# Kernel tuning notes

Hardware: AMD Instinct MI355X
Metric: run time of the kernel (lower is better)

Reference implementation:

```python
import jax, jax.numpy as jnp
import numpy as np

N_NODES = 40000
N_EDGES = 640000
D_IN = 512
D_OUT = 128


def setup_inputs() -> dict:
    key = jax.random.key(0)
    k_x, k_w, k_a, k_v, k_r, k_c = jax.random.split(key, 6)
    # Xavier-uniform bound for Linear(in=512, out=128)
    bound = float(np.sqrt(6.0 / (D_IN + D_OUT)))
    x = jax.random.normal(k_x, (N_NODES, D_IN), dtype=jnp.float32)
    weight = jax.random.uniform(k_w, (D_OUT, D_IN), dtype=jnp.float32,
                                minval=-bound, maxval=bound)
    bias = jnp.zeros((D_OUT,), dtype=jnp.float32)
    # PReLU default init is 0.25 (single shared slope)
    alpha = jnp.full((1,), 0.25, dtype=jnp.float32)
    edge_val = jax.random.uniform(k_v, (N_EDGES,), dtype=jnp.float32)
    edge_row = jax.random.randint(k_r, (N_EDGES,), 0, N_NODES, dtype=jnp.int32)
    edge_col = jax.random.randint(k_c, (N_EDGES,), 0, N_NODES, dtype=jnp.int32)
    return {"x": x, "weight": weight, "bias": bias, "alpha": alpha,
            "edge_val": edge_val, "edge_row": edge_row, "edge_col": edge_col}


def reference(x, weight, bias, alpha, edge_val, edge_row, edge_col):
    # seq = fc_1(input): [N, D_out]
    seq = jnp.einsum('ni,oi->no', x, weight)
    # torch.spmm(adj, seq) with adj in COO form:
    # out[r] = sum over edges (r, c, v) of v * seq[c]
    msgs = edge_val[:, None] * seq[edge_col]          # [E, D_out]
    agg = jax.ops.segment_sum(msgs, edge_row, num_segments=x.shape[0])
    agg = agg + bias
    # PReLU with a single shared slope alpha
    return jnp.where(agg > 0, agg, alpha[0] * agg)
```

## Files before the change

kernel.cpp:

```cpp
#include <hip/hip_runtime.h>
#include <hip/hip_bf16.h>

#define N_NODES 40000
#define N_EDGES 640000
#define D_IN 512
#define D_OUT 128
#define BM 128
#define BK 64
#define CAP 128
#define NB_GE 313
#define EPT 4
#define NB_SC 625

typedef __attribute__((ext_vector_type(4))) float f32x4;
typedef __attribute__((ext_vector_type(8))) short bf16x8;
typedef __attribute__((ext_vector_type(4))) unsigned short us4;

static __device__ __forceinline__ unsigned short f2bf(float f) {
    unsigned int u = __float_as_uint(f);
    unsigned int r = u + 0x7fffu + ((u >> 16) & 1u);
    return (unsigned short)(r >> 16);
}

__global__ void zero_kernel(int* __restrict__ p, int n) {
    int i = blockIdx.x * blockDim.x + threadIdx.x;
    if (i < n) p[i] = 0;
}

__global__ __launch_bounds__(256) void fused_kernel(
    const float* __restrict__ x, const float* __restrict__ w,
    unsigned short* __restrict__ seq,
    const int* __restrict__ erow, const int* __restrict__ ecol,
    const float* __restrict__ eval, int* __restrict__ cursor,
    float2* __restrict__ bucket)
{
    if (blockIdx.x >= NB_GE) {
        const int base = (blockIdx.x - NB_GE) * (256 * EPT) + threadIdx.x;
        int r[EPT], c[EPT];
        float v[EPT];
        #pragma unroll
        for (int k = 0; k < EPT; k++) {
            int e = base + k * 256;
            r[k] = erow[e]; c[k] = ecol[e]; v[k] = eval[e];
        }
        int slot[EPT];
        #pragma unroll
        for (int k = 0; k < EPT; k++) slot[k] = atomicAdd(&cursor[r[k]], 1);
        #pragma unroll
        for (int k = 0; k < EPT; k++)
            bucket[(size_t)r[k] * CAP + slot[k]] = make_float2(v[k], __int_as_float(c[k]));
        return;
    }

    __shared__ unsigned short As[BM * BK];
    __shared__ unsigned short Bs[D_OUT * BK];

    const int tid = threadIdx.x;
    const int lane = tid & 63;
    const int wv = tid >> 6;
    const int block_row = blockIdx.x * BM;
    const int srow = tid >> 3;
    const int scol = (tid & 7) * 8;

    f32x4 ra[4][2], rb[4][2];

    auto issue_loads = [&](int k0) {
        #pragma unroll
        for (int p = 0; p < 4; ++p) {
            int gr = block_row + srow + p * 32; if (gr >= N_NODES) gr = N_NODES - 1;
            const float* sa = x + (size_t)gr * D_IN + k0 + scol;
            ra[p][0] = *(const f32x4*)sa;
            ra[p][1] = *(const f32x4*)(sa + 4);
            const float* sb = w + (size_t)(srow + p * 32) * D_IN + k0 + scol;
            rb[p][0] = *(const f32x4*)sb;
            rb[p][1] = *(const f32x4*)(sb + 4);
        }
    };

    f32x4 acc[2][8];
    #pragma unroll
    for (int i = 0; i < 2; i++)
        #pragma unroll
        for (int j = 0; j < 8; j++)
            acc[i][j] = f32x4{0.f, 0.f, 0.f, 0.f};

    issue_loads(0);

    for (int kt = 0; kt < D_IN / BK; ++kt) {
        __syncthreads();
        #pragma unroll
        for (int p = 0; p < 4; ++p) {
            int r = srow + p * 32;
            us4 h0, h1, g0, g1;
            #pragma unroll
            for (int q = 0; q < 4; q++) {
                h0[q] = f2bf(ra[p][0][q]); h1[q] = f2bf(ra[p][1][q]);
                g0[q] = f2bf(rb[p][0][q]); g1[q] = f2bf(rb[p][1][q]);
            }
            int off = (r * (BK * 2) + scol * 2) ^ ((r & 7) << 4);
            *(us4*)((char*)As + off)     = h0;
            *(us4*)((char*)As + off + 8) = h1;
            *(us4*)((char*)Bs + off)     = g0;
            *(us4*)((char*)Bs + off + 8) = g1;
        }
        if (kt < D_IN / BK - 1) issue_loads((kt + 1) * BK);
        __syncthreads();

        #pragma unroll
        for (int ks = 0; ks < 2; ++ks) {
            const int kb = ks * 32 + (lane >> 4) * 8;
            bf16x8 a[2], b[8];
            #pragma unroll
            for (int m = 0; m < 2; m++) {
                int r = wv * 32 + m * 16 + (lane & 15);
                int off = (r * (BK * 2) + kb * 2) ^ ((r & 7) << 4);
                a[m] = *(const bf16x8*)((const char*)As + off);
            }
            #pragma unroll
            for (int n = 0; n < 8; n++) {
                int r = n * 16 + (lane & 15);
                int off = (r * (BK * 2) + kb * 2) ^ ((r & 7) << 4);
                b[n] = *(const bf16x8*)((const char*)Bs + off);
            }
            #pragma unroll
            for (int m = 0; m < 2; m++)
                #pragma unroll
                for (int n = 0; n < 8; n++)
                    acc[m][n] = __builtin_amdgcn_mfma_f32_16x16x32_bf16(a[m], b[n], acc[m][n], 0, 0, 0);
        }
    }

    #pragma unroll
    for (int m = 0; m < 2; m++) {
        #pragma unroll
        for (int r = 0; r < 4; r++) {
            int grow = block_row + wv * 32 + m * 16 + (lane >> 4) * 4 + r;
            if (grow < N_NODES) {
                #pragma unroll
                for (int n = 0; n < 8; n++) {
                    int col = n * 16 + (lane & 15);
                    seq[(size_t)grow * D_OUT + col] = f2bf(acc[m][n][r]);
                }
            }
        }
    }
}

__global__ __launch_bounds__(256) void agg_kernel(
    const unsigned short* __restrict__ seq, const int* __restrict__ cursor,
    const float2* __restrict__ bucket, const float* __restrict__ bias,
    const float* __restrict__ alpha, float* __restrict__ out)
{
    const int row = blockIdx.x * 4 + (threadIdx.x >> 6);
    const int lane = threadIdx.x & 63;
    const int cnt = cursor[row];
    const float2* b = bucket + (size_t)row * CAP;

    float a0 = 0.f, a1 = 0.f;
    int e = 0;
    for (; e + 4 <= cnt; e += 4) {
        float2 q0 = b[e], q1 = b[e + 1], q2 = b[e + 2], q3 = b[e + 3];
        unsigned int p0 = *(const unsigned int*)(seq + (size_t)__float_as_uint(q0.y) * D_OUT + lane * 2);
        unsigned int p1 = *(const unsigned int*)(seq + (size_t)__float_as_uint(q1.y) * D_OUT + lane * 2);
        unsigned int p2 = *(const unsigned int*)(seq + (size_t)__float_as_uint(q2.y) * D_OUT + lane * 2);
        unsigned int p3 = *(const unsigned int*)(seq + (size_t)__float_as_uint(q3.y) * D_OUT + lane * 2);
        a0 += q0.x * __uint_as_float(p0 << 16);
        a1 += q0.x * __uint_as_float(p0 & 0xffff0000u);
        a0 += q1.x * __uint_as_float(p1 << 16);
        a1 += q1.x * __uint_as_float(p1 & 0xffff0000u);
        a0 += q2.x * __uint_as_float(p2 << 16);
        a1 += q2.x * __uint_as_float(p2 & 0xffff0000u);
        a0 += q3.x * __uint_as_float(p3 << 16);
        a1 += q3.x * __uint_as_float(p3 & 0xffff0000u);
    }
    for (; e < cnt; ++e) {
        float2 q0 = b[e];
        unsigned int p0 = *(const unsigned int*)(seq + (size_t)__float_as_uint(q0.y) * D_OUT + lane * 2);
        a0 += q0.x * __uint_as_float(p0 << 16);
        a1 += q0.x * __uint_as_float(p0 & 0xffff0000u);
    }
    float al = alpha[0];
    float2 bi = *(const float2*)(bias + lane * 2);
    float r0 = a0 + bi.x;
    float r1 = a1 + bi.y;
    r0 = r0 > 0.f ? r0 : al * r0;
    r1 = r1 > 0.f ? r1 : al * r1;
    *(float2*)(out + (size_t)row * D_OUT + lane * 2) = make_float2(r0, r1);
}

extern "C" void kernel_launch(void* const* d_in, const int* in_sizes, int n_in,
                              void* d_out, int out_size, void* d_ws, size_t ws_size,
                              hipStream_t stream)
{
    (void)in_sizes; (void)n_in; (void)out_size; (void)ws_size;
    const float* x     = (const float*)d_in[0];
    const float* w     = (const float*)d_in[1];
    const float* bias  = (const float*)d_in[2];
    const float* alpha = (const float*)d_in[3];
    const float* eval  = (const float*)d_in[4];
    const int*   erow  = (const int*)d_in[5];
    const int*   ecol  = (const int*)d_in[6];
    float* out = (float*)d_out;

    char* ws = (char*)d_ws;
    unsigned short* seq = (unsigned short*)ws;
    int*    cursor = (int*)(ws + 10240000);
    float2* bucket = (float2*)(ws + 10400000);

    zero_kernel<<<(N_NODES + 255) / 256, 256, 0, stream>>>(cursor, N_NODES);
    fused_kernel<<<NB_GE + NB_SC, 256, 0, stream>>>(x, w, seq, erow, ecol, eval, cursor, bucket);
    agg_kernel<<<N_NODES / 4, 256, 0, stream>>>(seq, cursor, bucket, bias, alpha, out);
}
```

Baseline: 194.2 us.

## Pack edge buckets to 32-bit bf16+col, shrink capacity, add overflow list

Edge buckets are compacted from float2 (value, col) at 128 slots per row to a single 32-bit word holding the bf16 value and a 16-bit column, with 32 slots per row. Edges past that capacity go to a global overflow list that every aggregation wave scans linearly. The zeroing kernel now clears the whole bucket region as well, and the aggregation loop is unrolled by 8 over the zero-padded slots. This cuts bucket memory traffic but rounds edge values to bf16 and needs column indices below 65536. It also relies on the overflow list staying small; with on the order of 16 edges per row it should rarely be used.

```diff
diff --git a/kernel.cpp b/kernel.cpp
--- a/kernel.cpp
+++ b/kernel.cpp
@@ -7,10 +7,11 @@
 #define D_OUT 128
 #define BM 128
 #define BK 64
-#define CAP 128
+#define CAPC 32
+#define OVF_MAX 4096
 #define NB_GE 313
+#define NB_SC 625
 #define EPT 4
-#define NB_SC 625
 
 typedef __attribute__((ext_vector_type(4))) float f32x4;
 typedef __attribute__((ext_vector_type(8))) short bf16x8;
@@ -22,9 +23,11 @@
     return (unsigned short)(r >> 16);
 }
 
-__global__ void zero_kernel(int* __restrict__ p, int n) {
-    int i = blockIdx.x * blockDim.x + threadIdx.x;
-    if (i < n) p[i] = 0;
+__global__ __launch_bounds__(256) void prep_kernel(int4* __restrict__ zbase, int nz4)
+{
+    const int stride = 512 * 256;
+    for (int i = blockIdx.x * 256 + threadIdx.x; i < nz4; i += stride)
+        zbase[i] = make_int4(0, 0, 0, 0);
 }
 
 __global__ __launch_bounds__(256) void fused_kernel(
@@ -32,23 +35,32 @@
     unsigned short* __restrict__ seq,
     const int* __restrict__ erow, const int* __restrict__ ecol,
     const float* __restrict__ eval, int* __restrict__ cursor,
-    float2* __restrict__ bucket)
+    unsigned int* __restrict__ bucket, int* __restrict__ ovf_cnt,
+    int4* __restrict__ ovf)
 {
     if (blockIdx.x >= NB_GE) {
         const int base = (blockIdx.x - NB_GE) * (256 * EPT) + threadIdx.x;
         int r[EPT], c[EPT];
         float v[EPT];
         #pragma unroll
-        for (int k = 0; k < EPT; k++) {
-            int e = base + k * 256;
-            r[k] = erow[e]; c[k] = ecol[e]; v[k] = eval[e];
+        for (int j = 0; j < EPT; j++) {
+            int e = base + j * 256;
+            r[j] = erow[e]; c[j] = ecol[e]; v[j] = eval[e];
         }
         int slot[EPT];
         #pragma unroll
-        for (int k = 0; k < EPT; k++) slot[k] = atomicAdd(&cursor[r[k]], 1);
-        #pragma unroll
-        for (int k = 0; k < EPT; k++)
-            bucket[(size_t)r[k] * CAP + slot[k]] = make_float2(v[k], __int_as_float(c[k]));
+        for (int j = 0; j < EPT; j++) slot[j] = atomicAdd(&cursor[r[j]], 1);
+        #pragma unroll
+        for (int j = 0; j < EPT; j++) {
+            if (slot[j] < CAPC) {
+                bucket[(size_t)r[j] * CAPC + slot[j]] =
+                    ((unsigned int)f2bf(v[j]) << 16) | (unsigned int)c[j];
+            } else {
+                int o = atomicAdd(ovf_cnt, 1);
+                if (o < OVF_MAX)
+                    ovf[o] = make_int4(r[j], c[j], __float_as_int(v[j]), 0);
+            }
+        }
         return;
     }
 
@@ -148,37 +160,42 @@
 
 __global__ __launch_bounds__(256) void agg_kernel(
     const unsigned short* __restrict__ seq, const int* __restrict__ cursor,
-    const float2* __restrict__ bucket, const float* __restrict__ bias,
+    const unsigned int* __restrict__ bucket, const int* __restrict__ ovf_cnt,
+    const int4* __restrict__ ovf, const float* __restrict__ bias,
     const float* __restrict__ alpha, float* __restrict__ out)
 {
     const int row = blockIdx.x * 4 + (threadIdx.x >> 6);
     const int lane = threadIdx.x & 63;
-    const int cnt = cursor[row];
-    const float2* b = bucket + (size_t)row * CAP;
+
+    int cnt = cursor[row];
+    int mx = cnt < CAPC ? cnt : CAPC;
+    const unsigned int* bk = bucket + (size_t)row * CAPC;
 
     float a0 = 0.f, a1 = 0.f;
-    int e = 0;
-    for (; e + 4 <= cnt; e += 4) {
-        float2 q0 = b[e], q1 = b[e + 1], q2 = b[e + 2], q3 = b[e + 3];
-        unsigned int p0 = *(const unsigned int*)(seq + (size_t)__float_as_uint(q0.y) * D_OUT + lane * 2);
-        unsigned int p1 = *(const unsigned int*)(seq + (size_t)__float_as_uint(q1.y) * D_OUT + lane * 2);
-        unsigned int p2 = *(const unsigned int*)(seq + (size_t)__float_as_uint(q2.y) * D_OUT + lane * 2);
-        unsigned int p3 = *(const unsigned int*)(seq + (size_t)__float_as_uint(q3.y) * D_OUT + lane * 2);
-        a0 += q0.x * __uint_as_float(p0 << 16);
-        a1 += q0.x * __uint_as_float(p0 & 0xffff0000u);
-        a0 += q1.x * __uint_as_float(p1 << 16);
-        a1 += q1.x * __uint_as_float(p1 & 0xffff0000u);
-        a0 += q2.x * __uint_as_float(p2 << 16);
-        a1 += q2.x * __uint_as_float(p2 & 0xffff0000u);
-        a0 += q3.x * __uint_as_float(p3 << 16);
-        a1 += q3.x * __uint_as_float(p3 & 0xffff0000u);
-    }
-    for (; e < cnt; ++e) {
-        float2 q0 = b[e];
-        unsigned int p0 = *(const unsigned int*)(seq + (size_t)__float_as_uint(q0.y) * D_OUT + lane * 2);
-        a0 += q0.x * __uint_as_float(p0 << 16);
-        a1 += q0.x * __uint_as_float(p0 & 0xffff0000u);
-    }
+    for (int s = 0; s < mx; s += 8) {
+        #pragma unroll
+        for (int j = 0; j < 8; j++) {
+            unsigned int q = bk[s + j];
+            float vv = __uint_as_float(q & 0xffff0000u);
+            int col = q & 0xffff;
+            unsigned int p = *(const unsigned int*)(seq + ((size_t)col << 7) + lane * 2);
+            a0 += vv * __uint_as_float(p << 16);
+            a1 += vv * __uint_as_float(p & 0xffff0000u);
+        }
+    }
+
+    int on = *ovf_cnt;
+    on = on < OVF_MAX ? on : OVF_MAX;
+    for (int i = 0; i < on; ++i) {
+        int4 t = ovf[i];
+        if (t.x == row) {
+            float vv = __int_as_float(t.z);
+            unsigned int p = *(const unsigned int*)(seq + ((size_t)t.y << 7) + lane * 2);
+            a0 += vv * __uint_as_float(p << 16);
+            a1 += vv * __uint_as_float(p & 0xffff0000u);
+        }
+    }
+
     float al = alpha[0];
     float2 bi = *(const float2*)(bias + lane * 2);
     float r0 = a0 + bi.x;
@@ -203,11 +220,16 @@
     float* out = (float*)d_out;
 
     char* ws = (char*)d_ws;
-    unsigned short* seq = (unsigned short*)ws;
-    int*    cursor = (int*)(ws + 10240000);
-    float2* bucket = (float2*)(ws + 10400000);
-
-    zero_kernel<<<(N_NODES + 255) / 256, 256, 0, stream>>>(cursor, N_NODES);
-    fused_kernel<<<NB_GE + NB_SC, 256, 0, stream>>>(x, w, seq, erow, ecol, eval, cursor, bucket);
-    agg_kernel<<<N_NODES / 4, 256, 0, stream>>>(seq, cursor, bucket, bias, alpha, out);
-}
+    unsigned short* seq  = (unsigned short*)ws;
+    int*  cursor  = (int*)(ws + 10240000);
+    int*  ovf_cnt = (int*)(ws + 10400000);
+    int4* ovf     = (int4*)(ws + 10400016);
+    unsigned int* bucket = (unsigned int*)(ws + 10465552);
+
+    const int nz4 = 334097;
+    prep_kernel<<<512, 256, 0, stream>>>((int4*)(ws + 10240000), nz4);
+    fused_kernel<<<NB_GE + NB_SC, 256, 0, stream>>>(x, w, seq, erow, ecol, eval,
+                                                    cursor, bucket, ovf_cnt, ovf);
+    agg_kernel<<<N_NODES / 4, 256, 0, stream>>>(seq, cursor, bucket, ovf_cnt, ovf,
+                                                bias, alpha, out);
+}
```

New measurement: 189.2 us. 2.6% less time.
